# Optimization experiments

Measured on AMD Instinct MI355X. Metric: run time of the kernel, lower is better.

The kernel has to match this reference:

```python
import jax, jax.numpy as jnp
import numpy as np

B, D_INNER, D_STATE, DT_RANK = 1024, 2560, 16, 160


def setup_inputs() -> dict:
    key = jax.random.key(0)
    ks = jax.random.split(key, 9)
    s = lambda n: 1.0 / np.sqrt(n)
    return {
        "x": jax.random.normal(ks[0], (B, D_INNER), jnp.float32),
        "h": jax.random.normal(ks[1], (B, D_INNER, D_STATE), jnp.float32),
        "W_dt_low": jax.random.normal(ks[2], (DT_RANK, D_INNER), jnp.float32) * s(D_INNER),
        "W_dt": jax.random.normal(ks[3], (D_INNER, DT_RANK), jnp.float32) * s(DT_RANK),
        "b_dt": jax.random.normal(ks[4], (D_INNER,), jnp.float32),
        "W_B": jax.random.normal(ks[5], (D_STATE, D_INNER), jnp.float32) * s(D_INNER),
        "W_C": jax.random.normal(ks[6], (D_STATE, D_INNER), jnp.float32) * s(D_INNER),
        "A_log": jax.random.uniform(ks[7], (D_INNER, D_STATE), jnp.float32, 0.0, 1.0),
        "D": jax.random.normal(ks[8], (D_INNER,), jnp.float32),
    }


def reference(x, h, W_dt_low, W_dt, b_dt, W_B, W_C, A_log, D):
    # Single-token Mamba selective-scan step (decode).
    # dt projections: d_inner -> dt_rank -> d_inner, then softplus
    dt = jax.nn.softplus(jnp.einsum('bd,rd->br', x, W_dt_low) @ W_dt.T + b_dt)  # [B, D_INNER]
    Bt = jnp.einsum('bd,nd->bn', x, W_B)  # [B, D_STATE]
    Ct = jnp.einsum('bd,nd->bn', x, W_C)  # [B, D_STATE]
    A = -jnp.exp(A_log)                   # [D_INNER, D_STATE]
    delta_A = jnp.exp(dt[:, :, None] * A[None])                 # [B, D_INNER, D_STATE]
    delta_B_x = dt[:, :, None] * Bt[:, None, :] * x[:, :, None] # [B, D_INNER, D_STATE]
    h_new = delta_A * h + delta_B_x
    y = jnp.einsum('bdn,bn->bd', h_new, Ct) + D * x             # [B, D_INNER]
    return y
```

## Files before the change

kernel.cpp:

```cpp
#include <hip/hip_runtime.h>
#include <hip/hip_bf16.h>
#include <math.h>

#define B_SZ    1024
#define DI      2560
#define DS      16
#define DR      160
#define NPROJ   192

typedef __bf16 bf16x8 __attribute__((ext_vector_type(8)));
typedef float  f32x4  __attribute__((ext_vector_type(4)));

__global__ void __launch_bounds__(256) convert_kernel(
    const float* __restrict__ x, const float* __restrict__ Wdl,
    const float* __restrict__ WB, const float* __restrict__ WC,
    const float* __restrict__ Wdt, const float* __restrict__ A_log,
    __bf16* __restrict__ xb, __bf16* __restrict__ wcat,
    __bf16* __restrict__ wdtb, float* __restrict__ negA) {
  int i = blockIdx.x * 256 + threadIdx.x;
  const int NX   = B_SZ * DI;
  const int NWDL = DR * DI;
  const int NWB  = DS * DI;
  const int NWDT = DI * DR;
  const int NA   = DI * DS;
  if (i < NX)   { xb[i] = (__bf16)x[i]; return; }
  i -= NX;
  if (i < NWDL) { wcat[i] = (__bf16)Wdl[i]; return; }
  i -= NWDL;
  if (i < NWB)  { wcat[NWDL + i] = (__bf16)WB[i]; return; }
  i -= NWB;
  if (i < NWB)  { wcat[NWDL + NWB + i] = (__bf16)WC[i]; return; }
  i -= NWB;
  if (i < NWDT) { wdtb[i] = (__bf16)Wdt[i]; return; }
  i -= NWDT;
  if (i < NA)   { negA[i] = -__expf(A_log[i]); }
}

__global__ void __launch_bounds__(256) proj_kernel(
    const __bf16* __restrict__ xb, const __bf16* __restrict__ wcat,
    __bf16* __restrict__ dtlow, float* __restrict__ Bt, float* __restrict__ Ct) {
  int gw    = blockIdx.x * 4 + (threadIdx.x >> 6);
  int lane  = threadIdx.x & 63;
  int mtile = gw & 63;
  int ntile = gw >> 6;
  int b0 = mtile * 16, n0 = ntile * 16;
  int m = lane & 15, quad = lane >> 4;
  const __bf16* ap = xb   + (size_t)(b0 + m) * DI + quad * 8;
  const __bf16* bp = wcat + (size_t)(n0 + m) * DI + quad * 8;
  f32x4 acc = {0.f, 0.f, 0.f, 0.f};
  for (int k0 = 0; k0 < DI; k0 += 32) {
    bf16x8 a = *(const bf16x8*)(ap + k0);
    bf16x8 b = *(const bf16x8*)(bp + k0);
    acc = __builtin_amdgcn_mfma_f32_16x16x32_bf16(a, b, acc, 0, 0, 0);
  }
  int nn = n0 + m;
#pragma unroll
  for (int r = 0; r < 4; ++r) {
    int bb = b0 + quad * 4 + r;
    float v = acc[r];
    if (nn < DR)            dtlow[bb * DR + nn] = (__bf16)v;
    else if (nn < DR + DS)  Bt[bb * DS + (nn - DR)] = v;
    else                    Ct[bb * DS + (nn - DR - DS)] = v;
  }
}

__global__ void __launch_bounds__(256) dt_kernel(
    const __bf16* __restrict__ dtlow, const __bf16* __restrict__ wdtb,
    const float* __restrict__ b_dt, float* __restrict__ dt) {
  int gw    = blockIdx.x * 4 + (threadIdx.x >> 6);
  int lane  = threadIdx.x & 63;
  int mtile = gw & 63;
  int ntile = gw >> 6;
  int b0 = mtile * 16, d0 = ntile * 16;
  int m = lane & 15, quad = lane >> 4;
  const __bf16* ap = dtlow + (size_t)(b0 + m) * DR + quad * 8;
  const __bf16* bp = wdtb  + (size_t)(d0 + m) * DR + quad * 8;
  f32x4 acc = {0.f, 0.f, 0.f, 0.f};
#pragma unroll
  for (int k0 = 0; k0 < DR; k0 += 32) {
    bf16x8 a = *(const bf16x8*)(ap + k0);
    bf16x8 b = *(const bf16x8*)(bp + k0);
    acc = __builtin_amdgcn_mfma_f32_16x16x32_bf16(a, b, acc, 0, 0, 0);
  }
  int dd = d0 + m;
  float bias = b_dt[dd];
#pragma unroll
  for (int r = 0; r < 4; ++r) {
    int bb = b0 + quad * 4 + r;
    float z = acc[r] + bias;
    float sp = (z > 20.f) ? z : log1pf(__expf(z));
    dt[(size_t)bb * DI + dd] = sp;
  }
}

__global__ void __launch_bounds__(256) ssm_kernel(
    const float* __restrict__ x, const float* __restrict__ h,
    const float* __restrict__ dt, const float* __restrict__ negA,
    const float* __restrict__ Bt, const float* __restrict__ Ct,
    const float* __restrict__ Dp, float* __restrict__ y) {
  int e = blockIdx.x * 256 + threadIdx.x;
  int b = e / DI;
  int d = e - b * DI;
  float dtv = dt[e];
  float xv  = x[e];
  float dtl = dtv * 1.44269504f;
  float dxv = dtv * xv;
  const float4* h4 = (const float4*)(h    + (size_t)e * DS);
  const float4* a4 = (const float4*)(negA + (size_t)d * DS);
  const float4* b4 = (const float4*)(Bt   + (size_t)b * DS);
  const float4* c4 = (const float4*)(Ct   + (size_t)b * DS);
  float acc = 0.f;
#pragma unroll
  for (int j = 0; j < 4; ++j) {
    float4 hv = h4[j], av = a4[j], bv = b4[j], cv = c4[j];
    acc += (exp2f(av.x * dtl) * hv.x + bv.x * dxv) * cv.x;
    acc += (exp2f(av.y * dtl) * hv.y + bv.y * dxv) * cv.y;
    acc += (exp2f(av.z * dtl) * hv.z + bv.z * dxv) * cv.z;
    acc += (exp2f(av.w * dtl) * hv.w + bv.w * dxv) * cv.w;
  }
  y[e] = acc + Dp[d] * xv;
}

extern "C" void kernel_launch(void* const* d_in, const int* in_sizes, int n_in,
                              void* d_out, int out_size, void* d_ws, size_t ws_size,
                              hipStream_t stream) {
  const float* x     = (const float*)d_in[0];
  const float* h     = (const float*)d_in[1];
  const float* Wdl   = (const float*)d_in[2];
  const float* Wdt   = (const float*)d_in[3];
  const float* b_dt  = (const float*)d_in[4];
  const float* WB    = (const float*)d_in[5];
  const float* WC    = (const float*)d_in[6];
  const float* A_log = (const float*)d_in[7];
  const float* Dp    = (const float*)d_in[8];
  float* y = (float*)d_out;

  char* ws = (char*)d_ws;
  __bf16* xb    = (__bf16*)(ws);
  __bf16* wcat  = (__bf16*)(ws + 5242880);
  __bf16* wdtb  = (__bf16*)(ws + 6225920);
  float*  negA  = (float*) (ws + 7045120);
  __bf16* dtlow = (__bf16*)(ws + 7208960);
  float*  Bt    = (float*) (ws + 7536640);
  float*  Ct    = (float*) (ws + 7602176);
  float*  dt    = (float*) (ws + 7667712);
  if (ws_size < 18153472) return;

  convert_kernel<<<13920, 256, 0, stream>>>(x, Wdl, WB, WC, Wdt, A_log,
                                            xb, wcat, wdtb, negA);
  proj_kernel<<<192, 256, 0, stream>>>(xb, wcat, dtlow, Bt, Ct);
  dt_kernel<<<2560, 256, 0, stream>>>(dtlow, wdtb, b_dt, dt);
  ssm_kernel<<<10240, 256, 0, stream>>>(x, h, dt, negA, Bt, Ct, Dp, y);
}
```

Before: 292.8 us.

## Fuse dt GEMM epilogue with SSM update and vectorize conversion kernel

Merges the dt projection kernel and the SSM state kernel, so each MFMA output element computes softplus and then the full 16-state update and y directly, with no round trip of dt through global memory and one fewer launch. The conversion kernel now processes four elements per thread with float4 loads and bf16x4 stores. The trade-off is the fused kernel's access to h: each lane reads 64 contiguous bytes at a stride of DI*DS between rows, which may coalesce worse than the old fully linear per-thread layout. The conversion path also relies on every segment size being a multiple of four.

```diff
diff --git a/kernel.cpp b/kernel.cpp
--- a/kernel.cpp
+++ b/kernel.cpp
@@ -9,7 +9,15 @@
 #define NPROJ   192
 
 typedef __bf16 bf16x8 __attribute__((ext_vector_type(8)));
+typedef __bf16 bf16x4 __attribute__((ext_vector_type(4)));
 typedef float  f32x4  __attribute__((ext_vector_type(4)));
+
+__device__ __forceinline__ void cvt4(const float* __restrict__ s,
+                                     __bf16* __restrict__ d, int i) {
+  float4 v = *(const float4*)(s + i);
+  bf16x4 o = { (__bf16)v.x, (__bf16)v.y, (__bf16)v.z, (__bf16)v.w };
+  *(bf16x4*)(d + i) = o;
+}
 
 __global__ void __launch_bounds__(256) convert_kernel(
     const float* __restrict__ x, const float* __restrict__ Wdl,
@@ -17,23 +25,27 @@
     const float* __restrict__ Wdt, const float* __restrict__ A_log,
     __bf16* __restrict__ xb, __bf16* __restrict__ wcat,
     __bf16* __restrict__ wdtb, float* __restrict__ negA) {
-  int i = blockIdx.x * 256 + threadIdx.x;
+  int i = (blockIdx.x * 256 + threadIdx.x) * 4;
   const int NX   = B_SZ * DI;
   const int NWDL = DR * DI;
   const int NWB  = DS * DI;
   const int NWDT = DI * DR;
   const int NA   = DI * DS;
-  if (i < NX)   { xb[i] = (__bf16)x[i]; return; }
+  if (i < NX)   { cvt4(x, xb, i); return; }
   i -= NX;
-  if (i < NWDL) { wcat[i] = (__bf16)Wdl[i]; return; }
+  if (i < NWDL) { cvt4(Wdl, wcat, i); return; }
   i -= NWDL;
-  if (i < NWB)  { wcat[NWDL + i] = (__bf16)WB[i]; return; }
+  if (i < NWB)  { cvt4(WB, wcat + NWDL, i); return; }
   i -= NWB;
-  if (i < NWB)  { wcat[NWDL + NWB + i] = (__bf16)WC[i]; return; }
+  if (i < NWB)  { cvt4(WC, wcat + NWDL + NWB, i); return; }
   i -= NWB;
-  if (i < NWDT) { wdtb[i] = (__bf16)Wdt[i]; return; }
+  if (i < NWDT) { cvt4(Wdt, wdtb, i); return; }
   i -= NWDT;
-  if (i < NA)   { negA[i] = -__expf(A_log[i]); }
+  if (i < NA) {
+    float4 v = *(const float4*)(A_log + i);
+    float4 o = { -__expf(v.x), -__expf(v.y), -__expf(v.z), -__expf(v.w) };
+    *(float4*)(negA + i) = o;
+  }
 }
 
 __global__ void __launch_bounds__(256) proj_kernel(
@@ -64,9 +76,13 @@
   }
 }
 
-__global__ void __launch_bounds__(256) dt_kernel(
+__global__ void __launch_bounds__(256) dtssm_kernel(
     const __bf16* __restrict__ dtlow, const __bf16* __restrict__ wdtb,
-    const float* __restrict__ b_dt, float* __restrict__ dt) {
+    const float* __restrict__ b_dt,
+    const float* __restrict__ x, const float* __restrict__ h,
+    const float* __restrict__ negA, const float* __restrict__ Bt,
+    const float* __restrict__ Ct, const float* __restrict__ Dp,
+    float* __restrict__ y) {
   int gw    = blockIdx.x * 4 + (threadIdx.x >> 6);
   int lane  = threadIdx.x & 63;
   int mtile = gw & 63;
@@ -84,41 +100,52 @@
   }
   int dd = d0 + m;
   float bias = b_dt[dd];
+  float dval = Dp[dd];
+  const float4* a4 = (const float4*)(negA + (size_t)dd * DS);
+  float4 av0 = a4[0], av1 = a4[1], av2 = a4[2], av3 = a4[3];
 #pragma unroll
   for (int r = 0; r < 4; ++r) {
     int bb = b0 + quad * 4 + r;
+    size_t e = (size_t)bb * DI + dd;
     float z = acc[r] + bias;
-    float sp = (z > 20.f) ? z : log1pf(__expf(z));
-    dt[(size_t)bb * DI + dd] = sp;
+    float dtv = (z > 20.f) ? z : log1pf(__expf(z));
+    float xv  = x[e];
+    float dtl = dtv * 1.44269504f;
+    float dxv = dtv * xv;
+    const float4* h4 = (const float4*)(h  + e * DS);
+    const float4* b4 = (const float4*)(Bt + (size_t)bb * DS);
+    const float4* c4 = (const float4*)(Ct + (size_t)bb * DS);
+    float s = 0.f;
+    {
+      float4 hv = h4[0], bv = b4[0], cv = c4[0];
+      s += (exp2f(av0.x * dtl) * hv.x + bv.x * dxv) * cv.x;
+      s += (exp2f(av0.y * dtl) * hv.y + bv.y * dxv) * cv.y;
+      s += (exp2f(av0.z * dtl) * hv.z + bv.z * dxv) * cv.z;
+      s += (exp2f(av0.w * dtl) * hv.w + bv.w * dxv) * cv.w;
+    }
+    {
+      float4 hv = h4[1], bv = b4[1], cv = c4[1];
+      s += (exp2f(av1.x * dtl) * hv.x + bv.x * dxv) * cv.x;
+      s += (exp2f(av1.y * dtl) * hv.y + bv.y * dxv) * cv.y;
+      s += (exp2f(av1.z * dtl) * hv.z + bv.z * dxv) * cv.z;
+      s += (exp2f(av1.w * dtl) * hv.w + bv.w * dxv) * cv.w;
+    }
+    {
+      float4 hv = h4[2], bv = b4[2], cv = c4[2];
+      s += (exp2f(av2.x * dtl) * hv.x + bv.x * dxv) * cv.x;
+      s += (exp2f(av2.y * dtl) * hv.y + bv.y * dxv) * cv.y;
+      s += (exp2f(av2.z * dtl) * hv.z + bv.z * dxv) * cv.z;
+      s += (exp2f(av2.w * dtl) * hv.w + bv.w * dxv) * cv.w;
+    }
+    {
+      float4 hv = h4[3], bv = b4[3], cv = c4[3];
+      s += (exp2f(av3.x * dtl) * hv.x + bv.x * dxv) * cv.x;
+      s += (exp2f(av3.y * dtl) * hv.y + bv.y * dxv) * cv.y;
+      s += (exp2f(av3.z * dtl) * hv.z + bv.z * dxv) * cv.z;
+      s += (exp2f(av3.w * dtl) * hv.w + bv.w * dxv) * cv.w;
+    }
+    y[e] = s + dval * xv;
   }
-}
-
-__global__ void __launch_bounds__(256) ssm_kernel(
-    const float* __restrict__ x, const float* __restrict__ h,
-    const float* __restrict__ dt, const float* __restrict__ negA,
-    const float* __restrict__ Bt, const float* __restrict__ Ct,
-    const float* __restrict__ Dp, float* __restrict__ y) {
-  int e = blockIdx.x * 256 + threadIdx.x;
-  int b = e / DI;
-  int d = e - b * DI;
-  float dtv = dt[e];
-  float xv  = x[e];
-  float dtl = dtv * 1.44269504f;
-  float dxv = dtv * xv;
-  const float4* h4 = (const float4*)(h    + (size_t)e * DS);
-  const float4* a4 = (const float4*)(negA + (size_t)d * DS);
-  const float4* b4 = (const float4*)(Bt   + (size_t)b * DS);
-  const float4* c4 = (const float4*)(Ct   + (size_t)b * DS);
-  float acc = 0.f;
-#pragma unroll
-  for (int j = 0; j < 4; ++j) {
-    float4 hv = h4[j], av = a4[j], bv = b4[j], cv = c4[j];
-    acc += (exp2f(av.x * dtl) * hv.x + bv.x * dxv) * cv.x;
-    acc += (exp2f(av.y * dtl) * hv.y + bv.y * dxv) * cv.y;
-    acc += (exp2f(av.z * dtl) * hv.z + bv.z * dxv) * cv.z;
-    acc += (exp2f(av.w * dtl) * hv.w + bv.w * dxv) * cv.w;
-  }
-  y[e] = acc + Dp[d] * xv;
 }
 
 extern "C" void kernel_launch(void* const* d_in, const int* in_sizes, int n_in,
@@ -143,12 +170,11 @@
   __bf16* dtlow = (__bf16*)(ws + 7208960);
   float*  Bt    = (float*) (ws + 7536640);
   float*  Ct    = (float*) (ws + 7602176);
-  float*  dt    = (float*) (ws + 7667712);
-  if (ws_size < 18153472) return;
+  if (ws_size < 7667712) return;
 
-  convert_kernel<<<13920, 256, 0, stream>>>(x, Wdl, WB, WC, Wdt, A_log,
-                                            xb, wcat, wdtb, negA);
+  convert_kernel<<<3480, 256, 0, stream>>>(x, Wdl, WB, WC, Wdt, A_log,
+                                           xb, wcat, wdtb, negA);
   proj_kernel<<<192, 256, 0, stream>>>(xb, wcat, dtlow, Bt, Ct);
-  dt_kernel<<<2560, 256, 0, stream>>>(dtlow, wdtb, b_dt, dt);
-  ssm_kernel<<<10240, 256, 0, stream>>>(x, h, dt, negA, Bt, Ct, Dp, y);
+  dtssm_kernel<<<2560, 256, 0, stream>>>(dtlow, wdtb, b_dt, x, h, negA,
+                                         Bt, Ct, Dp, y);
 }
```

Result: faster. 286.9 us, median of 2 (-2.0%).
